# Kernel optimization log

Measured on AMD Instinct MI355X. Metric: run time of the kernel, lower is better.

## Reference

```python
import jax, jax.numpy as jnp
import numpy as np
from math import log2

B, F, C, H, W = 4, 16, 3, 96, 128
P = 8
HP, WP = H // P, W // P            # 12, 16
N = HP * WP                        # 192 spatial tokens
DIM, HEADS, DH = 512, 8, 64
INNER = HEADS * DH                 # 512
DEPTH = 4
FFH = DIM * 4                      # 2048 (GEGLU output half)
SCALE = DH ** -0.5


def _rotate_every_two(x):
    # pairs adjacent elements: (x0,x1) -> (-x1, x0)
    x1 = x[..., ::2]
    x2 = x[..., 1::2]
    return jnp.stack((-x2, x1), axis=-1).reshape(x.shape)


def _rope(t, sin, cos):
    return t * cos + _rotate_every_two(t) * sin


def _frame_rot():
    # RotaryEmbedding(DH): freqs concatenated (not interleaved)
    inv = 1.0 / (10000.0 ** (jnp.arange(0, DH, 2, dtype=jnp.float32) / DH))  # (32,)
    freqs = jnp.arange(F, dtype=jnp.float32)[:, None] * inv[None, :]          # (F,32)
    freqs = jnp.concatenate([freqs, freqs], axis=-1)                          # (F,64)
    return jnp.sin(freqs), jnp.cos(freqs)


def _image_rot():
    # AxialRotaryEmbedding(DH), max_freq=10; interleaved repeat (d j), j=2
    d4 = DH // 4
    scales = 2.0 ** jnp.linspace(0.0, log2(10.0 / 2.0), d4)                   # (16,)
    hs = jnp.linspace(-1.0, 1.0, HP)[:, None] * scales * jnp.pi              # (HP,16)
    ws = jnp.linspace(-1.0, 1.0, WP)[:, None] * scales * jnp.pi              # (WP,16)
    xs = jnp.broadcast_to(hs[:, None, :], (HP, WP, d4))
    ys = jnp.broadcast_to(ws[None, :, :], (HP, WP, d4))
    sin = jnp.concatenate([jnp.sin(xs), jnp.sin(ys)], axis=-1).reshape(N, DH // 2)
    cos = jnp.concatenate([jnp.cos(xs), jnp.cos(ys)], axis=-1).reshape(N, DH // 2)
    return jnp.repeat(sin, 2, axis=-1), jnp.repeat(cos, 2, axis=-1)           # (N,64)


def _ln(x, g, b):
    mu = x.mean(-1, keepdims=True)
    var = ((x - mu) ** 2).mean(-1, keepdims=True)
    return (x - mu) * jax.lax.rsqrt(var + 1e-5) * g + b


def _split_heads(t):
    # (B, F*N, HEADS*DH) -> (B, HEADS, F, N, DH); head dim is outer in (h d)
    return t.reshape(B, F, N, HEADS, DH).transpose(0, 3, 1, 2, 4)


def _merge_heads(t):
    # (B, HEADS, F, N, DH) -> (B, F*N, HEADS*DH)
    return t.transpose(0, 2, 3, 1, 4).reshape(B, F * N, INNER)


def _attention(y, wqkv, wo, bo, sin, cos, over_time):
    q, k, v = jnp.split(y @ wqkv, 3, axis=-1)
    q = q * SCALE
    q, k, v = map(_split_heads, (q, k, v))  # (B,h,F,N,DH)
    if over_time:
        s, c = sin[:, None, :], cos[:, None, :]     # broadcast over N
        q, k = _rope(q, s, c), _rope(k, s, c)
        sim = jnp.einsum('bhind,bhjnd->bhnij', q, k)
        a = jax.nn.softmax(sim, axis=-1)
        o = jnp.einsum('bhnij,bhjnd->bhind', a, v)
    else:
        q, k = _rope(q, sin, cos), _rope(k, sin, cos)  # sin/cos (N,DH)
        sim = jnp.einsum('bhfid,bhfjd->bhfij', q, k)
        a = jax.nn.softmax(sim, axis=-1)
        o = jnp.einsum('bhfij,bhfjd->bhfid', a, v)
    return _merge_heads(o) @ wo + bo


def _forward(video, patch_w, patch_b, ln_t_g, ln_t_b, ln_s_g, ln_s_b,
             ln_f_g, ln_f_b, qkv_t, out_t_w, out_t_b, qkv_s, out_s_w,
             out_s_b, ff_w1, ff_b1, ff_w2, ff_b2):
    # patchify: b f c (hp p1) (wp p2) -> b (f hp wp) (p1 p2 c)
    v = video.reshape(B, F, C, HP, P, WP, P).transpose(0, 1, 3, 5, 4, 6, 2)
    v = v.reshape(B, F * N, P * P * C)
    x = v @ patch_w + patch_b                       # (B, F*N, DIM)

    fsin, fcos = _frame_rot()
    isin, icos = _image_rot()

    for l in range(DEPTH):
        y = _ln(x, ln_t_g[l], ln_t_b[l])
        x = x + _attention(y, qkv_t[l], out_t_w[l], out_t_b[l], fsin, fcos, True)
        y = _ln(x, ln_s_g[l], ln_s_b[l])
        x = x + _attention(y, qkv_s[l], out_s_w[l], out_s_b[l], isin, icos, False)
        y = _ln(x, ln_f_g[l], ln_f_b[l])
        h1 = y @ ff_w1[l] + ff_b1[l]
        a, g = jnp.split(h1, 2, axis=-1)
        x = x + (a * jax.nn.gelu(g, approximate=False)) @ ff_w2[l] + ff_b2[l]
    return x


def setup_inputs() -> dict:
    key = jax.random.key(0)
    ks = jax.random.split(key, 10)
    s = 0.02
    return {
        'video': jax.random.normal(ks[0], (B, F, C, H, W), jnp.float32),
        'patch_w': jax.random.normal(ks[1], (C * P * P, DIM), jnp.float32) * s,
        'patch_b': jnp.zeros((DIM,), jnp.float32),
        'ln_t_g': jnp.ones((DEPTH, DIM), jnp.float32),
        'ln_t_b': jnp.zeros((DEPTH, DIM), jnp.float32),
        'ln_s_g': jnp.ones((DEPTH, DIM), jnp.float32),
        'ln_s_b': jnp.zeros((DEPTH, DIM), jnp.float32),
        'ln_f_g': jnp.ones((DEPTH, DIM), jnp.float32),
        'ln_f_b': jnp.zeros((DEPTH, DIM), jnp.float32),
        'qkv_t': jax.random.normal(ks[2], (DEPTH, DIM, 3 * INNER), jnp.float32) * s,
        'out_t_w': jax.random.normal(ks[3], (DEPTH, INNER, DIM), jnp.float32) * s,
        'out_t_b': jnp.zeros((DEPTH, DIM), jnp.float32),
        'qkv_s': jax.random.normal(ks[4], (DEPTH, DIM, 3 * INNER), jnp.float32) * s,
        'out_s_w': jax.random.normal(ks[5], (DEPTH, INNER, DIM), jnp.float32) * s,
        'out_s_b': jnp.zeros((DEPTH, DIM), jnp.float32),
        'ff_w1': jax.random.normal(ks[6], (DEPTH, DIM, 2 * FFH), jnp.float32) * s,
        'ff_b1': jnp.zeros((DEPTH, 2 * FFH), jnp.float32),
        'ff_w2': jax.random.normal(ks[7], (DEPTH, FFH, DIM), jnp.float32) * s,
        'ff_b2': jnp.zeros((DEPTH, DIM), jnp.float32),
    }


def reference(video, patch_w, patch_b, ln_t_g, ln_t_b, ln_s_g, ln_s_b,
              ln_f_g, ln_f_b, qkv_t, out_t_w, out_t_b, qkv_s, out_s_w,
              out_s_b, ff_w1, ff_b1, ff_w2, ff_b2):
    return _forward(video, patch_w, patch_b, ln_t_g, ln_t_b, ln_s_g, ln_s_b,
                    ln_f_g, ln_f_b, qkv_t, out_t_w, out_t_b, qkv_s, out_s_w,
                    out_s_b, ff_w1, ff_b1, ff_w2, ff_b2)
```

## Files before the change

kernel.cpp:

```cpp
#include <hip/hip_runtime.h>
#include <math.h>

#define B_ 4
#define F_ 16
#define HP_ 12
#define WP_ 16
#define N_ 192
#define S_ (F_*N_)
#define ROWS (B_*S_)
#define DIM_ 512
#define HEADS_ 8
#define DH_ 64
#define FFH_ 2048
#define PATCH_K 192
#define PI_F 3.14159265358979323846f

typedef unsigned short u16;
typedef __attribute__((ext_vector_type(8))) short bf16x8;
typedef __attribute__((ext_vector_type(4))) float f32x4;

__device__ __forceinline__ u16 bf16_rne(float f) {
    unsigned int u = __float_as_uint(f);
    u += 0x7FFFu + ((u >> 16) & 1u);
    return (u16)(u >> 16);
}
__device__ __forceinline__ float bf16_f32(u16 h) {
    return __uint_as_float(((unsigned int)h) << 16);
}

__global__ void rope_tables(float* __restrict__ fsin, float* __restrict__ fcos,
                            float* __restrict__ isin, float* __restrict__ icos) {
    int tid = blockIdx.x * blockDim.x + threadIdx.x;
    int stride = gridDim.x * blockDim.x;
    for (int idx = tid; idx < F_ * 64; idx += stride) {
        int f = idx >> 6, j = idx & 63;
        int i = j & 31;
        float inv = powf(10000.0f, -((float)i) / 32.0f);
        float fr = (float)f * inv;
        fsin[idx] = sinf(fr);
        fcos[idx] = cosf(fr);
    }
    for (int idx = tid; idx < N_ * 32; idx += stride) {
        int n = idx >> 5, k = idx & 31;
        int h = n / WP_, w = n % WP_;
        float scale = exp2f((float)(k & 15) * (log2f(5.0f) / 15.0f));
        float pos = (k < 16) ? (-1.0f + 2.0f * (float)h / (float)(HP_ - 1))
                             : (-1.0f + 2.0f * (float)w / (float)(WP_ - 1));
        float val = pos * scale * PI_F;
        float sv = sinf(val), cv = cosf(val);
        isin[n * 64 + 2 * k] = sv; isin[n * 64 + 2 * k + 1] = sv;
        icos[n * 64 + 2 * k] = cv; icos[n * 64 + 2 * k + 1] = cv;
    }
}

__global__ void rearrange_video_p(const float* __restrict__ video,
                                  u16* __restrict__ Vh, u16* __restrict__ Vl) {
    int t = blockIdx.x * blockDim.x + threadIdx.x;
    const int total = ROWS * PATCH_K;
    if (t >= total) return;
    int col = t % PATCH_K;
    int row = t / PATCH_K;
    int c  = col % 3;
    int pp = col / 3;
    int pi = pp >> 3, pj = pp & 7;
    int n  = row % N_;
    int bf = row / N_;
    int hp = n / WP_, wp = n % WP_;
    int hidx = hp * 8 + pi, widx = wp * 8 + pj;
    float f = video[((size_t)(bf * 3 + c) * 96 + hidx) * 128 + widx];
    u16 h = bf16_rne(f);
    Vh[t] = h;
    Vl[t] = bf16_rne(f - bf16_f32(h));
}

__global__ __launch_bounds__(256) void convert_wt(
    const float* __restrict__ W, u16* __restrict__ Wh, u16* __restrict__ Wl,
    int K, int N) {
    __shared__ float tile[32][33];
    int nb = blockIdx.x * 32, kb = blockIdx.y * 32;
    int tx = threadIdx.x & 31, ty = threadIdx.x >> 5;
    #pragma unroll
    for (int i = 0; i < 32; i += 8)
        tile[ty + i][tx] = W[(size_t)(kb + ty + i) * N + nb + tx];
    __syncthreads();
    #pragma unroll
    for (int i = 0; i < 32; i += 8) {
        int n = nb + ty + i, k = kb + tx;
        float f = tile[tx][ty + i];
        u16 h = bf16_rne(f);
        Wh[(size_t)n * K + k] = h;
        Wl[(size_t)n * K + k] = bf16_rne(f - bf16_f32(h));
    }
}

__global__ __launch_bounds__(64) void layernorm_p(
    const float* __restrict__ x, const float* __restrict__ g,
    const float* __restrict__ b, u16* __restrict__ Yh, u16* __restrict__ Yl) {
    int row = blockIdx.x;
    int lane = threadIdx.x;
    const float* xr = x + (size_t)row * DIM_;
    float4 v0 = *(const float4*)&xr[lane * 8];
    float4 v1 = *(const float4*)&xr[lane * 8 + 4];
    float s  = v0.x + v0.y + v0.z + v0.w + v1.x + v1.y + v1.z + v1.w;
    float sq = v0.x*v0.x + v0.y*v0.y + v0.z*v0.z + v0.w*v0.w
             + v1.x*v1.x + v1.y*v1.y + v1.z*v1.z + v1.w*v1.w;
    for (int off = 32; off; off >>= 1) { s += __shfl_xor(s, off); sq += __shfl_xor(sq, off); }
    float mu  = s * (1.0f / 512.0f);
    float var = sq * (1.0f / 512.0f) - mu * mu;
    float inv = rsqrtf(var + 1e-5f);
    float4 g0 = *(const float4*)&g[lane * 8];
    float4 g1 = *(const float4*)&g[lane * 8 + 4];
    float4 b0 = *(const float4*)&b[lane * 8];
    float4 b1 = *(const float4*)&b[lane * 8 + 4];
    float o[8];
    o[0] = (v0.x - mu) * inv * g0.x + b0.x;
    o[1] = (v0.y - mu) * inv * g0.y + b0.y;
    o[2] = (v0.z - mu) * inv * g0.z + b0.z;
    o[3] = (v0.w - mu) * inv * g0.w + b0.w;
    o[4] = (v1.x - mu) * inv * g1.x + b1.x;
    o[5] = (v1.y - mu) * inv * g1.y + b1.y;
    o[6] = (v1.z - mu) * inv * g1.z + b1.z;
    o[7] = (v1.w - mu) * inv * g1.w + b1.w;
    size_t ro = (size_t)row * DIM_ + lane * 8;
    ushort4 h0, h1, l0, l1;
    h0.x = bf16_rne(o[0]); l0.x = bf16_rne(o[0] - bf16_f32(h0.x));
    h0.y = bf16_rne(o[1]); l0.y = bf16_rne(o[1] - bf16_f32(h0.y));
    h0.z = bf16_rne(o[2]); l0.z = bf16_rne(o[2] - bf16_f32(h0.z));
    h0.w = bf16_rne(o[3]); l0.w = bf16_rne(o[3] - bf16_f32(h0.w));
    h1.x = bf16_rne(o[4]); l1.x = bf16_rne(o[4] - bf16_f32(h1.x));
    h1.y = bf16_rne(o[5]); l1.y = bf16_rne(o[5] - bf16_f32(h1.y));
    h1.z = bf16_rne(o[6]); l1.z = bf16_rne(o[6] - bf16_f32(h1.z));
    h1.w = bf16_rne(o[7]); l1.w = bf16_rne(o[7] - bf16_f32(h1.w));
    *(ushort4*)&Yh[ro]     = h0;
    *(ushort4*)&Yh[ro + 4] = h1;
    *(ushort4*)&Yl[ro]     = l0;
    *(ushort4*)&Yl[ro + 4] = l1;
}

template<int EPI>
__global__ __launch_bounds__(256) void gemm_mfma3(
    const u16* __restrict__ Ah, const u16* __restrict__ Al,
    const u16* __restrict__ Wh, const u16* __restrict__ Wl,
    const float* __restrict__ bias, float* __restrict__ C,
    int M, int N, int K) {
    __shared__ u16 As[2][128 * 40];
    __shared__ u16 Ws[2][128 * 40];
    const int bm0 = blockIdx.y * 128, bn0 = blockIdx.x * 128;
    const int tid = threadIdx.x, lane = tid & 63, wid = tid >> 6;
    const int wm = (wid >> 1) * 64, wn = (wid & 1) * 64;
    const int fr = lane & 15, kg = (lane >> 4) * 8;
    f32x4 acc[4][4] = {};
    for (int k0 = 0; k0 < K; k0 += 32) {
        #pragma unroll
        for (int it = 0; it < 2; ++it) {
            int cc = it * 256 + tid;
            int row = cc >> 2, kc = (cc & 3) * 8;
            size_t ga = (size_t)(bm0 + row) * K + k0 + kc;
            size_t gw = (size_t)(bn0 + row) * K + k0 + kc;
            *(uint4*)&As[0][row * 40 + kc] = *(const uint4*)&Ah[ga];
            *(uint4*)&As[1][row * 40 + kc] = *(const uint4*)&Al[ga];
            *(uint4*)&Ws[0][row * 40 + kc] = *(const uint4*)&Wh[gw];
            *(uint4*)&Ws[1][row * 40 + kc] = *(const uint4*)&Wl[gw];
        }
        __syncthreads();
        bf16x8 ah[4], al[4], bh[4], bl[4];
        #pragma unroll
        for (int i = 0; i < 4; ++i) {
            ah[i] = *(const bf16x8*)&As[0][(wm + i * 16 + fr) * 40 + kg];
            al[i] = *(const bf16x8*)&As[1][(wm + i * 16 + fr) * 40 + kg];
            bh[i] = *(const bf16x8*)&Ws[0][(wn + i * 16 + fr) * 40 + kg];
            bl[i] = *(const bf16x8*)&Ws[1][(wn + i * 16 + fr) * 40 + kg];
        }
        #pragma unroll
        for (int i = 0; i < 4; ++i)
            #pragma unroll
            for (int j = 0; j < 4; ++j) {
                acc[i][j] = __builtin_amdgcn_mfma_f32_16x16x32_bf16(ah[i], bh[j], acc[i][j], 0, 0, 0);
                acc[i][j] = __builtin_amdgcn_mfma_f32_16x16x32_bf16(ah[i], bl[j], acc[i][j], 0, 0, 0);
                acc[i][j] = __builtin_amdgcn_mfma_f32_16x16x32_bf16(al[i], bh[j], acc[i][j], 0, 0, 0);
            }
        __syncthreads();
    }
    const int r0 = (lane >> 4) * 4;
    #pragma unroll
    for (int i = 0; i < 4; ++i)
        #pragma unroll
        for (int j = 0; j < 4; ++j) {
            int col = bn0 + wn + j * 16 + fr;
            float bb = bias ? bias[col] : 0.0f;
            #pragma unroll
            for (int r = 0; r < 4; ++r) {
                int row = bm0 + wm + i * 16 + r0 + r;
                float v = acc[i][j][r] + bb;
                size_t off = (size_t)row * N + col;
                if (EPI == 1) v += C[off];
                C[off] = v;
            }
        }
}

__global__ __launch_bounds__(256) void gemm_glu3(
    const u16* __restrict__ Ah, const u16* __restrict__ Al,
    const u16* __restrict__ Wh, const u16* __restrict__ Wl,
    const float* __restrict__ bias, u16* __restrict__ Hh, u16* __restrict__ Hl) {
    const int K = DIM_;
    __shared__ u16 As[2][128 * 40];
    __shared__ u16 Ws[2][128 * 40];
    const int bm0 = blockIdx.y * 128, bn0 = blockIdx.x * 64;
    const int tid = threadIdx.x, lane = tid & 63, wid = tid >> 6;
    const int wm = (wid >> 1) * 64, wn2 = (wid & 1) * 32;
    const int fr = lane & 15, kg = (lane >> 4) * 8;
    f32x4 acca[4][2] = {}, accg[4][2] = {};
    for (int k0 = 0; k0 < K; k0 += 32) {
        #pragma unroll
        for (int it = 0; it < 2; ++it) {
            int cc = it * 256 + tid;
            int row = cc >> 2, kc = (cc & 3) * 8;
            size_t ga = (size_t)(bm0 + row) * K + k0 + kc;
            int ng = (row < 64) ? (bn0 + row) : (FFH_ + bn0 + row - 64);
            size_t gw = (size_t)ng * K + k0 + kc;
            *(uint4*)&As[0][row * 40 + kc] = *(const uint4*)&Ah[ga];
            *(uint4*)&As[1][row * 40 + kc] = *(const uint4*)&Al[ga];
            *(uint4*)&Ws[0][row * 40 + kc] = *(const uint4*)&Wh[gw];
            *(uint4*)&Ws[1][row * 40 + kc] = *(const uint4*)&Wl[gw];
        }
        __syncthreads();
        bf16x8 ah[4], al[4], bah[2], bal[2], bgh[2], bgl[2];
        #pragma unroll
        for (int i = 0; i < 4; ++i) {
            ah[i] = *(const bf16x8*)&As[0][(wm + i * 16 + fr) * 40 + kg];
            al[i] = *(const bf16x8*)&As[1][(wm + i * 16 + fr) * 40 + kg];
        }
        #pragma unroll
        for (int j = 0; j < 2; ++j) {
            bah[j] = *(const bf16x8*)&Ws[0][(wn2 + j * 16 + fr) * 40 + kg];
            bal[j] = *(const bf16x8*)&Ws[1][(wn2 + j * 16 + fr) * 40 + kg];
            bgh[j] = *(const bf16x8*)&Ws[0][(64 + wn2 + j * 16 + fr) * 40 + kg];
            bgl[j] = *(const bf16x8*)&Ws[1][(64 + wn2 + j * 16 + fr) * 40 + kg];
        }
        #pragma unroll
        for (int i = 0; i < 4; ++i)
            #pragma unroll
            for (int j = 0; j < 2; ++j) {
                acca[i][j] = __builtin_amdgcn_mfma_f32_16x16x32_bf16(ah[i], bah[j], acca[i][j], 0, 0, 0);
                acca[i][j] = __builtin_amdgcn_mfma_f32_16x16x32_bf16(ah[i], bal[j], acca[i][j], 0, 0, 0);
                acca[i][j] = __builtin_amdgcn_mfma_f32_16x16x32_bf16(al[i], bah[j], acca[i][j], 0, 0, 0);
                accg[i][j] = __builtin_amdgcn_mfma_f32_16x16x32_bf16(ah[i], bgh[j], accg[i][j], 0, 0, 0);
                accg[i][j] = __builtin_amdgcn_mfma_f32_16x16x32_bf16(ah[i], bgl[j], accg[i][j], 0, 0, 0);
                accg[i][j] = __builtin_amdgcn_mfma_f32_16x16x32_bf16(al[i], bgh[j], accg[i][j], 0, 0, 0);
            }
        __syncthreads();
    }
    const int r0 = (lane >> 4) * 4;
    #pragma unroll
    for (int i = 0; i < 4; ++i)
        #pragma unroll
        for (int j = 0; j < 2; ++j) {
            int col = bn0 + wn2 + j * 16 + fr;
            float ba = bias[col], bg = bias[FFH_ + col];
            #pragma unroll
            for (int r = 0; r < 4; ++r) {
                int row = bm0 + wm + i * 16 + r0 + r;
                float av = acca[i][j][r] + ba;
                float gv = accg[i][j][r] + bg;
                float gl = 0.5f * gv * (1.0f + erff(gv * 0.70710678118654752f));
                float v = av * gl;
                u16 h = bf16_rne(v);
                size_t off = (size_t)row * FFH_ + col;
                Hh[off] = h;
                Hl[off] = bf16_rne(v - bf16_f32(h));
            }
        }
}

__global__ __launch_bounds__(64) void attn_time(
    const float* __restrict__ qkv, const float* __restrict__ fsin,
    const float* __restrict__ fcos, u16* __restrict__ Oh, u16* __restrict__ Ol) {
    int bid = blockIdx.x;
    int n = bid % N_;
    int h = (bid / N_) % HEADS_;
    int b = bid / (N_ * HEADS_);
    int lane = threadIdx.x;
    __shared__ float qs[16][68], ks[16][68], vs[16][68], Pm[16][16];
    int parity = lane & 1;
    for (int f = 0; f < F_; ++f) {
        size_t base = (size_t)(b * S_ + f * N_ + n) * 1536 + h * 64;
        float qv = qkv[base + lane] * 0.125f;
        float kv = qkv[base + 512 + lane];
        float vv = qkv[base + 1024 + lane];
        float sn = fsin[f * 64 + lane], cs = fcos[f * 64 + lane];
        float qx = __shfl_xor(qv, 1);
        float kx = __shfl_xor(kv, 1);
        float qrot = parity ? qx : -qx;
        float krot = parity ? kx : -kx;
        qs[f][lane] = qv * cs + qrot * sn;
        ks[f][lane] = kv * cs + krot * sn;
        vs[f][lane] = vv;
    }
    __syncthreads();
    int j = lane & 15, r = lane >> 4;
    for (int rr = 0; rr < 4; ++rr) {
        int i = rr * 4 + r;
        float sacc = 0.f;
        #pragma unroll
        for (int d4 = 0; d4 < 16; ++d4) {
            float4 qa = *(const float4*)&qs[i][d4 * 4];
            float4 ka = *(const float4*)&ks[j][d4 * 4];
            sacc += qa.x*ka.x + qa.y*ka.y + qa.z*ka.z + qa.w*ka.w;
        }
        float mx = sacc;
        for (int off = 8; off; off >>= 1) mx = fmaxf(mx, __shfl_xor(mx, off));
        float p = expf(sacc - mx);
        float sum = p;
        for (int off = 8; off; off >>= 1) sum += __shfl_xor(sum, off);
        Pm[i][j] = p / sum;
    }
    __syncthreads();
    for (int i = 0; i < 16; ++i) {
        float acc = 0.f;
        #pragma unroll
        for (int jj = 0; jj < 16; ++jj) acc += Pm[i][jj] * vs[jj][lane];
        size_t ob = (size_t)(b * S_ + i * N_ + n) * 512 + h * 64 + lane;
        u16 hh = bf16_rne(acc);
        Oh[ob] = hh;
        Ol[ob] = bf16_rne(acc - bf16_f32(hh));
    }
}

__global__ __launch_bounds__(256, 2) void attn_space_mfma(
    const float* __restrict__ qkv, const float* __restrict__ isin,
    const float* __restrict__ icos, u16* __restrict__ Oh, u16* __restrict__ Ol) {
    int bid = blockIdx.x;
    int f = bid % F_;
    int h = (bid / F_) % HEADS_;
    int b = bid / (F_ * HEADS_);
    const int tid = threadIdx.x, lane = tid & 63, wid = tid >> 6;
    const int fr = lane & 15, g = lane >> 4;
    __shared__ u16 Ksh[32][72], Ksl[32][72];
    __shared__ u16 Vsh[64][40], Vsl[64][40];
    __shared__ u16 Psh[4][48][40], Psl[4][48][40];
    const size_t rowbase = (size_t)b * S_ + (size_t)f * N_;

    bf16x8 qh[3][2], ql[3][2];
    #pragma unroll
    for (int i = 0; i < 3; ++i) {
        int n = wid * 48 + i * 16 + fr;
        #pragma unroll
        for (int ks = 0; ks < 2; ++ks) {
            int dbase = ks * 32 + g * 8;
            const float* qp = &qkv[(rowbase + n) * 1536 + h * 64 + dbase];
            float4 t0 = *(const float4*)qp;
            float4 t1 = *(const float4*)(qp + 4);
            float4 s0 = *(const float4*)&isin[n * 64 + dbase];
            float4 s1 = *(const float4*)&isin[n * 64 + dbase + 4];
            float4 c0 = *(const float4*)&icos[n * 64 + dbase];
            float4 c1 = *(const float4*)&icos[n * 64 + dbase + 4];
            float v[8];
            v[0] = (t0.x * c0.x - t0.y * s0.x) * 0.125f;
            v[1] = (t0.y * c0.y + t0.x * s0.y) * 0.125f;
            v[2] = (t0.z * c0.z - t0.w * s0.z) * 0.125f;
            v[3] = (t0.w * c0.w + t0.z * s0.w) * 0.125f;
            v[4] = (t1.x * c1.x - t1.y * s1.x) * 0.125f;
            v[5] = (t1.y * c1.y + t1.x * s1.y) * 0.125f;
            v[6] = (t1.z * c1.z - t1.w * s1.z) * 0.125f;
            v[7] = (t1.w * c1.w + t1.z * s1.w) * 0.125f;
            bf16x8 hh, ll;
            #pragma unroll
            for (int e = 0; e < 8; ++e) {
                u16 hb = bf16_rne(v[e]);
                hh[e] = (short)hb;
                ll[e] = (short)bf16_rne(v[e] - bf16_f32(hb));
            }
            qh[i][ks] = hh; ql[i][ks] = ll;
        }
    }

    float m[3][4], l[3][4];
    f32x4 oacc[3][4] = {};
    #pragma unroll
    for (int i = 0; i < 3; ++i)
        #pragma unroll
        for (int r = 0; r < 4; ++r) { m[i][r] = -3.0e38f; l[i][r] = 0.0f; }

    for (int kt = 0; kt < 6; ++kt) {
        __syncthreads();
        #pragma unroll
        for (int it = 0; it < 2; ++it) {
            int c = it * 256 + tid;
            int kr = c >> 4, dseg = (c & 15) * 4;
            int nk = kt * 32 + kr;
            float4 t = *(const float4*)&qkv[(rowbase + nk) * 1536 + 512 + h * 64 + dseg];
            float4 sn = *(const float4*)&isin[nk * 64 + dseg];
            float4 cs = *(const float4*)&icos[nk * 64 + dseg];
            float v0 = t.x * cs.x - t.y * sn.x;
            float v1 = t.y * cs.y + t.x * sn.y;
            float v2 = t.z * cs.z - t.w * sn.z;
            float v3 = t.w * cs.w + t.z * sn.w;
            ushort4 hh, ll;
            hh.x = bf16_rne(v0); ll.x = bf16_rne(v0 - bf16_f32(hh.x));
            hh.y = bf16_rne(v1); ll.y = bf16_rne(v1 - bf16_f32(hh.y));
            hh.z = bf16_rne(v2); ll.z = bf16_rne(v2 - bf16_f32(hh.z));
            hh.w = bf16_rne(v3); ll.w = bf16_rne(v3 - bf16_f32(hh.w));
            *(ushort4*)&Ksh[kr][dseg] = hh;
            *(ushort4*)&Ksl[kr][dseg] = ll;
        }
        {
            int kr = tid & 31, ds8 = tid >> 5;
            const float* vp = &qkv[(rowbase + kt * 32 + kr) * 1536 + 1024 + h * 64 + ds8 * 8];
            float4 a = *(const float4*)vp;
            float4 b4 = *(const float4*)(vp + 4);
            float vv[8] = {a.x, a.y, a.z, a.w, b4.x, b4.y, b4.z, b4.w};
            #pragma unroll
            for (int e = 0; e < 8; ++e) {
                u16 hb = bf16_rne(vv[e]);
                Vsh[ds8 * 8 + e][kr] = hb;
                Vsl[ds8 * 8 + e][kr] = bf16_rne(vv[e] - bf16_f32(hb));
            }
        }
        __syncthreads();
        bf16x8 kbh[2][2], kbl[2][2];
        #pragma unroll
        for (int j = 0; j < 2; ++j)
            #pragma unroll
            for (int ks = 0; ks < 2; ++ks) {
                kbh[j][ks] = *(const bf16x8*)&Ksh[j * 16 + fr][ks * 32 + g * 8];
                kbl[j][ks] = *(const bf16x8*)&Ksl[j * 16 + fr][ks * 32 + g * 8];
            }
        f32x4 s[3][2] = {};
        #pragma unroll
        for (int i = 0; i < 3; ++i)
            #pragma unroll
            for (int j = 0; j < 2; ++j)
                #pragma unroll
                for (int ks = 0; ks < 2; ++ks) {
                    s[i][j] = __builtin_amdgcn_mfma_f32_16x16x32_bf16(qh[i][ks], kbh[j][ks], s[i][j], 0, 0, 0);
                    s[i][j] = __builtin_amdgcn_mfma_f32_16x16x32_bf16(qh[i][ks], kbl[j][ks], s[i][j], 0, 0, 0);
                    s[i][j] = __builtin_amdgcn_mfma_f32_16x16x32_bf16(ql[i][ks], kbh[j][ks], s[i][j], 0, 0, 0);
                }
        #pragma unroll
        for (int i = 0; i < 3; ++i) {
            float tmax[4], mn[4], corr[4], psum[4];
            #pragma unroll
            for (int r = 0; r < 4; ++r) tmax[r] = fmaxf(s[i][0][r], s[i][1][r]);
            #pragma unroll
            for (int off = 8; off; off >>= 1)
                #pragma unroll
                for (int r = 0; r < 4; ++r) tmax[r] = fmaxf(tmax[r], __shfl_xor(tmax[r], off));
            float p0[4], p1[4];
            #pragma unroll
            for (int r = 0; r < 4; ++r) {
                mn[r] = fmaxf(m[i][r], tmax[r]);
                corr[r] = expf(m[i][r] - mn[r]);
                p0[r] = expf(s[i][0][r] - mn[r]);
                p1[r] = expf(s[i][1][r] - mn[r]);
                psum[r] = p0[r] + p1[r];
                m[i][r] = mn[r];
            }
            #pragma unroll
            for (int off = 8; off; off >>= 1)
                #pragma unroll
                for (int r = 0; r < 4; ++r) psum[r] += __shfl_xor(psum[r], off);
            #pragma unroll
            for (int r = 0; r < 4; ++r) l[i][r] = l[i][r] * corr[r] + psum[r];
            #pragma unroll
            for (int dj = 0; dj < 4; ++dj)
                #pragma unroll
                for (int r = 0; r < 4; ++r) oacc[i][dj][r] *= corr[r];
            #pragma unroll
            for (int r = 0; r < 4; ++r) {
                int rl = i * 16 + g * 4 + r;
                u16 h0 = bf16_rne(p0[r]);
                Psh[wid][rl][fr]      = h0;
                Psl[wid][rl][fr]      = bf16_rne(p0[r] - bf16_f32(h0));
                u16 h1 = bf16_rne(p1[r]);
                Psh[wid][rl][16 + fr] = h1;
                Psl[wid][rl][16 + fr] = bf16_rne(p1[r] - bf16_f32(h1));
            }
        }
        bf16x8 pah[3], pal[3];
        #pragma unroll
        for (int i = 0; i < 3; ++i) {
            pah[i] = *(const bf16x8*)&Psh[wid][i * 16 + fr][g * 8];
            pal[i] = *(const bf16x8*)&Psl[wid][i * 16 + fr][g * 8];
        }
        bf16x8 vbh[4], vbl[4];
        #pragma unroll
        for (int dj = 0; dj < 4; ++dj) {
            vbh[dj] = *(const bf16x8*)&Vsh[dj * 16 + fr][g * 8];
            vbl[dj] = *(const bf16x8*)&Vsl[dj * 16 + fr][g * 8];
        }
        #pragma unroll
        for (int i = 0; i < 3; ++i)
            #pragma unroll
            for (int dj = 0; dj < 4; ++dj) {
                oacc[i][dj] = __builtin_amdgcn_mfma_f32_16x16x32_bf16(pah[i], vbh[dj], oacc[i][dj], 0, 0, 0);
                oacc[i][dj] = __builtin_amdgcn_mfma_f32_16x16x32_bf16(pah[i], vbl[dj], oacc[i][dj], 0, 0, 0);
                oacc[i][dj] = __builtin_amdgcn_mfma_f32_16x16x32_bf16(pal[i], vbh[dj], oacc[i][dj], 0, 0, 0);
            }
    }
    #pragma unroll
    for (int i = 0; i < 3; ++i) {
        #pragma unroll
        for (int r = 0; r < 4; ++r) {
            int row = wid * 48 + i * 16 + g * 4 + r;
            float invl = 1.0f / l[i][r];
            #pragma unroll
            for (int dj = 0; dj < 4; ++dj) {
                float v = oacc[i][dj][r] * invl;
                size_t ob = (rowbase + row) * 512 + h * 64 + dj * 16 + fr;
                u16 hh = bf16_rne(v);
                Oh[ob] = hh;
                Ol[ob] = bf16_rne(v - bf16_f32(hh));
            }
        }
    }
}

extern "C" void kernel_launch(void* const* d_in, const int* in_sizes, int n_in,
                              void* d_out, int out_size, void* d_ws, size_t ws_size,
                              hipStream_t stream) {
    (void)in_sizes; (void)n_in; (void)out_size; (void)ws_size;
    const float* video   = (const float*)d_in[0];
    const float* patch_w = (const float*)d_in[1];
    const float* patch_b = (const float*)d_in[2];
    const float* ln_t_g  = (const float*)d_in[3];
    const float* ln_t_b  = (const float*)d_in[4];
    const float* ln_s_g  = (const float*)d_in[5];
    const float* ln_s_b  = (const float*)d_in[6];
    const float* ln_f_g  = (const float*)d_in[7];
    const float* ln_f_b  = (const float*)d_in[8];
    const float* qkv_t   = (const float*)d_in[9];
    const float* out_t_w = (const float*)d_in[10];
    const float* out_t_b = (const float*)d_in[11];
    const float* qkv_s   = (const float*)d_in[12];
    const float* out_s_w = (const float*)d_in[13];
    const float* out_s_b = (const float*)d_in[14];
    const float* ff_w1   = (const float*)d_in[15];
    const float* ff_b1   = (const float*)d_in[16];
    const float* ff_w2   = (const float*)d_in[17];
    const float* ff_b2   = (const float*)d_in[18];

    float* x = (float*)d_out;

    u16* wqt_h = (u16*)d_ws;
    u16* wqt_l = wqt_h + 1536 * 512;
    u16* wot_h = wqt_l + 1536 * 512;
    u16* wot_l = wot_h + 512 * 512;
    u16* wqs_h = wot_l + 512 * 512;
    u16* wqs_l = wqs_h + 1536 * 512;
    u16* wos_h = wqs_l + 1536 * 512;
    u16* wos_l = wos_h + 512 * 512;
    u16* wpt_h = wos_l + 512 * 512;
    u16* wpt_l = wpt_h + 512 * PATCH_K;
    u16* y_h   = wpt_l + 512 * PATCH_K;
    u16* y_l   = y_h + (size_t)ROWS * DIM_;
    float* big2 = (float*)(y_l + (size_t)ROWS * DIM_);
    float* qkv  = big2;
    u16* vp_h = (u16*)big2;
    u16* vp_l = vp_h + (size_t)ROWS * PATCH_K;
    u16* h2_h = (u16*)big2;
    u16* h2_l = h2_h + (size_t)(ROWS / 2) * FFH_;
    u16* f1t_h = h2_l + (size_t)(ROWS / 2) * FFH_;
    u16* f1t_l = f1t_h + 4096 * 512;
    u16* f2t_h = f1t_l + 4096 * 512;
    u16* f2t_l = f2t_h + 512 * FFH_;
    float* fsin = (float*)((char*)big2 + (size_t)ROWS * 1536 * 4);
    float* fcos = fsin + F_ * 64;
    float* isin = fcos + F_ * 64;
    float* icos = isin + N_ * 64;
    u16* o_h = y_h;
    u16* o_l = y_l;

    rope_tables<<<2, 256, 0, stream>>>(fsin, fcos, isin, icos);

    convert_wt<<<dim3(DIM_ / 32, PATCH_K / 32), 256, 0, stream>>>(patch_w, wpt_h, wpt_l, PATCH_K, DIM_);
    rearrange_video_p<<<(ROWS * PATCH_K + 255) / 256, 256, 0, stream>>>(video, vp_h, vp_l);
    gemm_mfma3<0><<<dim3(DIM_ / 128, ROWS / 128), 256, 0, stream>>>(
        vp_h, vp_l, wpt_h, wpt_l, patch_b, x, ROWS, DIM_, PATCH_K);

    for (int l = 0; l < 4; ++l) {
        convert_wt<<<dim3(1536 / 32, DIM_ / 32), 256, 0, stream>>>(
            qkv_t + (size_t)l * DIM_ * 1536, wqt_h, wqt_l, DIM_, 1536);
        convert_wt<<<dim3(DIM_ / 32, DIM_ / 32), 256, 0, stream>>>(
            out_t_w + (size_t)l * DIM_ * DIM_, wot_h, wot_l, DIM_, DIM_);
        convert_wt<<<dim3(1536 / 32, DIM_ / 32), 256, 0, stream>>>(
            qkv_s + (size_t)l * DIM_ * 1536, wqs_h, wqs_l, DIM_, 1536);
        convert_wt<<<dim3(DIM_ / 32, DIM_ / 32), 256, 0, stream>>>(
            out_s_w + (size_t)l * DIM_ * DIM_, wos_h, wos_l, DIM_, DIM_);

        layernorm_p<<<ROWS, 64, 0, stream>>>(x, ln_t_g + l * DIM_, ln_t_b + l * DIM_, y_h, y_l);
        gemm_mfma3<0><<<dim3(1536 / 128, ROWS / 128), 256, 0, stream>>>(
            y_h, y_l, wqt_h, wqt_l, nullptr, qkv, ROWS, 1536, DIM_);
        attn_time<<<B_ * HEADS_ * N_, 64, 0, stream>>>(qkv, fsin, fcos, o_h, o_l);
        gemm_mfma3<1><<<dim3(DIM_ / 128, ROWS / 128), 256, 0, stream>>>(
            o_h, o_l, wot_h, wot_l, out_t_b + l * DIM_, x, ROWS, DIM_, DIM_);

        layernorm_p<<<ROWS, 64, 0, stream>>>(x, ln_s_g + l * DIM_, ln_s_b + l * DIM_, y_h, y_l);
        gemm_mfma3<0><<<dim3(1536 / 128, ROWS / 128), 256, 0, stream>>>(
            y_h, y_l, wqs_h, wqs_l, nullptr, qkv, ROWS, 1536, DIM_);
        attn_space_mfma<<<B_ * HEADS_ * F_, 256, 0, stream>>>(qkv, isin, icos, o_h, o_l);
        gemm_mfma3<1><<<dim3(DIM_ / 128, ROWS / 128), 256, 0, stream>>>(
            o_h, o_l, wos_h, wos_l, out_s_b + l * DIM_, x, ROWS, DIM_, DIM_);

        convert_wt<<<dim3(4096 / 32, DIM_ / 32), 256, 0, stream>>>(
            ff_w1 + (size_t)l * DIM_ * 2 * FFH_, f1t_h, f1t_l, DIM_, 4096);
        convert_wt<<<dim3(DIM_ / 32, FFH_ / 32), 256, 0, stream>>>(
            ff_w2 + (size_t)l * FFH_ * DIM_, f2t_h, f2t_l, FFH_, DIM_);
        layernorm_p<<<ROWS, 64, 0, stream>>>(x, ln_f_g + l * DIM_, ln_f_b + l * DIM_, y_h, y_l);
        const int MH = ROWS / 2;
        for (int half = 0; half < 2; ++half) {
            const u16* yh = y_h + (size_t)half * MH * DIM_;
            const u16* yl = y_l + (size_t)half * MH * DIM_;
            float*     xh = x   + (size_t)half * MH * DIM_;
            gemm_glu3<<<dim3(FFH_ / 64, MH / 128), 256, 0, stream>>>(
                yh, yl, f1t_h, f1t_l, ff_b1 + l * 2 * FFH_, h2_h, h2_l);
            gemm_mfma3<1><<<dim3(DIM_ / 128, MH / 128), 256, 0, stream>>>(
                h2_h, h2_l, f2t_h, f2t_l, ff_b2 + l * DIM_, xh, MH, DIM_, FFH_);
        }
    }
}
```

Baseline: 3.105 ms.

## Add N64 GEMM tiles, block swizzle, and single-bf16 GLU hidden activations

Adds a 2D block-index swizzle to the GEMM kernels, aimed at better L2 locality. Adds a new 128x64-tile GEMM that doubles block count for the N=512 projections. The GEGLU hidden activations are now stored as plain bf16 instead of a hi/lo split, which drops one MFMA term in the FF2 GEMM and halves that buffer. The FF is also run over all rows in one pass instead of two halves, cutting launches. Dropping the low-order part of the hidden activations lowers precision and could affect accuracy tolerance.

```diff
diff --git a/kernel.cpp b/kernel.cpp
--- a/kernel.cpp
+++ b/kernel.cpp
@@ -26,6 +26,18 @@
 }
 __device__ __forceinline__ float bf16_f32(u16 h) {
     return __uint_as_float(((unsigned int)h) << 16);
+}
+
+__device__ __forceinline__ void swz2d(int& bx, int& by) {
+    int gx = gridDim.x;
+    int nwg = gx * gridDim.y;
+    int id = by * gx + bx;
+    if ((nwg & 7) == 0) {
+        int cpx = nwg >> 3;
+        int wg = (id & 7) * cpx + (id >> 3);
+        bx = wg % gx;
+        by = wg / gx;
+    }
 }
 
 __global__ void rope_tables(float* __restrict__ fsin, float* __restrict__ fcos,
@@ -145,7 +157,9 @@
     int M, int N, int K) {
     __shared__ u16 As[2][128 * 40];
     __shared__ u16 Ws[2][128 * 40];
-    const int bm0 = blockIdx.y * 128, bn0 = blockIdx.x * 128;
+    int bx = blockIdx.x, by = blockIdx.y;
+    swz2d(bx, by);
+    const int bm0 = by * 128, bn0 = bx * 128;
     const int tid = threadIdx.x, lane = tid & 63, wid = tid >> 6;
     const int wm = (wid >> 1) * 64, wn = (wid & 1) * 64;
     const int fr = lane & 15, kg = (lane >> 4) * 8;
@@ -199,14 +213,89 @@
         }
 }
 
+template<int EPI, int SPLITA>
+__global__ __launch_bounds__(256) void gemm_n64(
+    const u16* __restrict__ Ah, const u16* __restrict__ Al,
+    const u16* __restrict__ Wh, const u16* __restrict__ Wl,
+    const float* __restrict__ bias, float* __restrict__ C,
+    int M, int N, int K) {
+    __shared__ u16 As[SPLITA ? 2 : 1][128 * 40];
+    __shared__ u16 Ws[2][64 * 40];
+    int bx = blockIdx.x, by = blockIdx.y;
+    swz2d(bx, by);
+    const int bm0 = by * 128, bn0 = bx * 64;
+    const int tid = threadIdx.x, lane = tid & 63, wid = tid >> 6;
+    const int wm = (wid >> 1) * 64, wn = (wid & 1) * 32;
+    const int fr = lane & 15, kg = (lane >> 4) * 8;
+    f32x4 acc[4][2] = {};
+    for (int k0 = 0; k0 < K; k0 += 32) {
+        #pragma unroll
+        for (int it = 0; it < 2; ++it) {
+            int cc = it * 256 + tid;
+            int row = cc >> 2, kc = (cc & 3) * 8;
+            size_t ga = (size_t)(bm0 + row) * K + k0 + kc;
+            *(uint4*)&As[0][row * 40 + kc] = *(const uint4*)&Ah[ga];
+            if (SPLITA)
+                *(uint4*)&As[1][row * 40 + kc] = *(const uint4*)&Al[ga];
+        }
+        {
+            int row = tid >> 2, kc = (tid & 3) * 8;
+            size_t gw = (size_t)(bn0 + row) * K + k0 + kc;
+            *(uint4*)&Ws[0][row * 40 + kc] = *(const uint4*)&Wh[gw];
+            *(uint4*)&Ws[1][row * 40 + kc] = *(const uint4*)&Wl[gw];
+        }
+        __syncthreads();
+        bf16x8 ah[4], al[4], bh[2], bl[2];
+        #pragma unroll
+        for (int i = 0; i < 4; ++i) {
+            ah[i] = *(const bf16x8*)&As[0][(wm + i * 16 + fr) * 40 + kg];
+            if (SPLITA)
+                al[i] = *(const bf16x8*)&As[1][(wm + i * 16 + fr) * 40 + kg];
+        }
+        #pragma unroll
+        for (int j = 0; j < 2; ++j) {
+            bh[j] = *(const bf16x8*)&Ws[0][(wn + j * 16 + fr) * 40 + kg];
+            bl[j] = *(const bf16x8*)&Ws[1][(wn + j * 16 + fr) * 40 + kg];
+        }
+        #pragma unroll
+        for (int i = 0; i < 4; ++i)
+            #pragma unroll
+            for (int j = 0; j < 2; ++j) {
+                acc[i][j] = __builtin_amdgcn_mfma_f32_16x16x32_bf16(ah[i], bh[j], acc[i][j], 0, 0, 0);
+                acc[i][j] = __builtin_amdgcn_mfma_f32_16x16x32_bf16(ah[i], bl[j], acc[i][j], 0, 0, 0);
+                if (SPLITA)
+                    acc[i][j] = __builtin_amdgcn_mfma_f32_16x16x32_bf16(al[i], bh[j], acc[i][j], 0, 0, 0);
+            }
+        __syncthreads();
+    }
+    const int r0 = (lane >> 4) * 4;
+    #pragma unroll
+    for (int i = 0; i < 4; ++i)
+        #pragma unroll
+        for (int j = 0; j < 2; ++j) {
+            int col = bn0 + wn + j * 16 + fr;
+            float bb = bias ? bias[col] : 0.0f;
+            #pragma unroll
+            for (int r = 0; r < 4; ++r) {
+                int row = bm0 + wm + i * 16 + r0 + r;
+                float v = acc[i][j][r] + bb;
+                size_t off = (size_t)row * N + col;
+                if (EPI == 1) v += C[off];
+                C[off] = v;
+            }
+        }
+}
+
 __global__ __launch_bounds__(256) void gemm_glu3(
     const u16* __restrict__ Ah, const u16* __restrict__ Al,
     const u16* __restrict__ Wh, const u16* __restrict__ Wl,
-    const float* __restrict__ bias, u16* __restrict__ Hh, u16* __restrict__ Hl) {
+    const float* __restrict__ bias, u16* __restrict__ Hh) {
     const int K = DIM_;
     __shared__ u16 As[2][128 * 40];
     __shared__ u16 Ws[2][128 * 40];
-    const int bm0 = blockIdx.y * 128, bn0 = blockIdx.x * 64;
+    int bx = blockIdx.x, by = blockIdx.y;
+    swz2d(bx, by);
+    const int bm0 = by * 128, bn0 = bx * 64;
     const int tid = threadIdx.x, lane = tid & 63, wid = tid >> 6;
     const int wm = (wid >> 1) * 64, wn2 = (wid & 1) * 32;
     const int fr = lane & 15, kg = (lane >> 4) * 8;
@@ -264,11 +353,7 @@
                 float av = acca[i][j][r] + ba;
                 float gv = accg[i][j][r] + bg;
                 float gl = 0.5f * gv * (1.0f + erff(gv * 0.70710678118654752f));
-                float v = av * gl;
-                u16 h = bf16_rne(v);
-                size_t off = (size_t)row * FFH_ + col;
-                Hh[off] = h;
-                Hl[off] = bf16_rne(v - bf16_f32(h));
+                Hh[(size_t)row * FFH_ + col] = bf16_rne(av * gl);
             }
         }
 }
@@ -558,9 +643,8 @@
     float* qkv  = big2;
     u16* vp_h = (u16*)big2;
     u16* vp_l = vp_h + (size_t)ROWS * PATCH_K;
-    u16* h2_h = (u16*)big2;
-    u16* h2_l = h2_h + (size_t)(ROWS / 2) * FFH_;
-    u16* f1t_h = h2_l + (size_t)(ROWS / 2) * FFH_;
+    u16* h2    = (u16*)big2;
+    u16* f1t_h = h2 + (size_t)ROWS * FFH_;
     u16* f1t_l = f1t_h + 4096 * 512;
     u16* f2t_h = f1t_l + 4096 * 512;
     u16* f2t_l = f2t_h + 512 * FFH_;
@@ -575,7 +659,7 @@
 
     convert_wt<<<dim3(DIM_ / 32, PATCH_K / 32), 256, 0, stream>>>(patch_w, wpt_h, wpt_l, PATCH_K, DIM_);
     rearrange_video_p<<<(ROWS * PATCH_K + 255) / 256, 256, 0, stream>>>(video, vp_h, vp_l);
-    gemm_mfma3<0><<<dim3(DIM_ / 128, ROWS / 128), 256, 0, stream>>>(
+    gemm_n64<0, 1><<<dim3(DIM_ / 64, ROWS / 128), 256, 0, stream>>>(
         vp_h, vp_l, wpt_h, wpt_l, patch_b, x, ROWS, DIM_, PATCH_K);
 
     for (int l = 0; l < 4; ++l) {
@@ -592,14 +676,14 @@
         gemm_mfma3<0><<<dim3(1536 / 128, ROWS / 128), 256, 0, stream>>>(
             y_h, y_l, wqt_h, wqt_l, nullptr, qkv, ROWS, 1536, DIM_);
         attn_time<<<B_ * HEADS_ * N_, 64, 0, stream>>>(qkv, fsin, fcos, o_h, o_l);
-        gemm_mfma3<1><<<dim3(DIM_ / 128, ROWS / 128), 256, 0, stream>>>(
+        gemm_n64<1, 1><<<dim3(DIM_ / 64, ROWS / 128), 256, 0, stream>>>(
             o_h, o_l, wot_h, wot_l, out_t_b + l * DIM_, x, ROWS, DIM_, DIM_);
 
         layernorm_p<<<ROWS, 64, 0, stream>>>(x, ln_s_g + l * DIM_, ln_s_b + l * DIM_, y_h, y_l);
         gemm_mfma3<0><<<dim3(1536 / 128, ROWS / 128), 256, 0, stream>>>(
             y_h, y_l, wqs_h, wqs_l, nullptr, qkv, ROWS, 1536, DIM_);
         attn_space_mfma<<<B_ * HEADS_ * F_, 256, 0, stream>>>(qkv, isin, icos, o_h, o_l);
-        gemm_mfma3<1><<<dim3(DIM_ / 128, ROWS / 128), 256, 0, stream>>>(
+        gemm_n64<1, 1><<<dim3(DIM_ / 64, ROWS / 128), 256, 0, stream>>>(
             o_h, o_l, wos_h, wos_l, out_s_b + l * DIM_, x, ROWS, DIM_, DIM_);
 
         convert_wt<<<dim3(4096 / 32, DIM_ / 32), 256, 0, stream>>>(
@@ -607,15 +691,9 @@
         convert_wt<<<dim3(DIM_ / 32, FFH_ / 32), 256, 0, stream>>>(
             ff_w2 + (size_t)l * FFH_ * DIM_, f2t_h, f2t_l, FFH_, DIM_);
         layernorm_p<<<ROWS, 64, 0, stream>>>(x, ln_f_g + l * DIM_, ln_f_b + l * DIM_, y_h, y_l);
-        const int MH = ROWS / 2;
-        for (int half = 0; half < 2; ++half) {
-            const u16* yh = y_h + (size_t)half * MH * DIM_;
-            const u16* yl = y_l + (size_t)half * MH * DIM_;
-            float*     xh = x   + (size_t)half * MH * DIM_;
-            gemm_glu3<<<dim3(FFH_ / 64, MH / 128), 256, 0, stream>>>(
-                yh, yl, f1t_h, f1t_l, ff_b1 + l * 2 * FFH_, h2_h, h2_l);
-            gemm_mfma3<1><<<dim3(DIM_ / 128, MH / 128), 256, 0, stream>>>(
-                h2_h, h2_l, f2t_h, f2t_l, ff_b2 + l * DIM_, xh, MH, DIM_, FFH_);
-        }
-    }
-}
+        gemm_glu3<<<dim3(FFH_ / 64, ROWS / 128), 256, 0, stream>>>(
+            y_h, y_l, f1t_h, f1t_l, ff_b1 + l * 2 * FFH_, h2);
+        gemm_n64<1, 0><<<dim3(DIM_ / 64, ROWS / 128), 256, 0, stream>>>(
+            h2, nullptr, f2t_h, f2t_l, ff_b2 + l * DIM_, x, ROWS, DIM_, FFH_);
+    }
+}
```

Result: faster. 2.542 ms (-18.1%).
